# Kernel optimization log

Hardware: AMD Instinct MI355X
Metric: run time of the kernel (lower is better)

## Reference

```python
import jax, jax.numpy as jnp
import numpy as np

HID = 2048      # hidden_size
H = 16          # num query heads
KV = 4          # num kv heads
HD = HID // H   # head_dim = 128
THETA = 1000000.0
T = 2048        # tokens (single causal sequence)


def _rope(x, positions):
    # neox-style rotate-half RoPE over full head_dim. x: [T, h, HD]
    half = HD // 2
    inv_freq = THETA ** (-jnp.arange(half, dtype=jnp.float32) * 2.0 / HD)  # [half]
    freqs = positions.astype(jnp.float32)[:, None] * inv_freq              # [T, half]
    cos = jnp.cos(freqs)[:, None, :]
    sin = jnp.sin(freqs)[:, None, :]
    x1, x2 = x[..., :half], x[..., half:]
    return jnp.concatenate([x1 * cos - x2 * sin, x2 * cos + x1 * sin], axis=-1)


def setup_inputs() -> dict:
    key = jax.random.key(0)
    k1, k2, k3 = jax.random.split(key, 3)
    hidden_states = jax.random.normal(k1, (T, HID), jnp.float32) * 0.02
    w_qkv = jax.random.normal(k2, (HID, (H + 2 * KV) * HD), jnp.float32) * 0.02
    w_o = jax.random.normal(k3, (H * HD, HID), jnp.float32) * 0.02
    positions = jnp.arange(T, dtype=jnp.int32)
    return {"hidden_states": hidden_states, "w_qkv": w_qkv, "w_o": w_o,
            "positions": positions}


def reference(hidden_states, w_qkv, w_o, positions):
    q_size, kv_size = H * HD, KV * HD
    qkv = hidden_states @ w_qkv                                  # [T, q+2kv]
    q = qkv[:, :q_size].reshape(T, H, HD)
    k = qkv[:, q_size:q_size + kv_size].reshape(T, KV, HD)
    v = qkv[:, q_size + kv_size:].reshape(T, KV, HD)
    q = _rope(q, positions)
    k = _rope(k, positions)
    # GQA: expand kv heads to query heads
    group = H // KV
    k_e = jnp.repeat(k, group, axis=1)                           # [T, H, HD]
    v_e = jnp.repeat(v, group, axis=1)
    scale = HD ** -0.5
    scores = jnp.einsum('thd,shd->hts', q, k_e) * scale          # [H, T, T]
    causal = positions[:, None] >= positions[None, :]            # [T, T]
    scores = jnp.where(causal[None, :, :], scores, -1e30)
    attn = jax.nn.softmax(scores, axis=-1)
    o = jnp.einsum('hts,shd->thd', attn, v_e).reshape(T, H * HD)
    return o @ w_o
```

## Files before the change

kernel.cpp:

```cpp
#include <hip/hip_runtime.h>
#include <hip/hip_bf16.h>

#define T_LEN 2048
#define HID 2048
#define NH 16
#define NKV 4
#define HD 128
#define QKV_COLS 3072

typedef __attribute__((ext_vector_type(8))) short bf16x8;
typedef __attribute__((ext_vector_type(4))) float f32x4;

static __device__ __forceinline__ ushort f2bf(float f) {
  __hip_bfloat16 h = __float2bfloat16(f);
  return *reinterpret_cast<ushort*>(&h);
}
static __device__ __forceinline__ float bf2f(ushort u) {
  union { unsigned int i; float f; } v;
  v.i = ((unsigned int)u) << 16;
  return v.f;
}

static __device__ __forceinline__ void async_copy16(const ushort* g, ushort* l) {
  __builtin_amdgcn_global_load_lds(
      (const __attribute__((address_space(1))) unsigned int*)g,
      (__attribute__((address_space(3))) unsigned int*)l, 16, 0, 0);
}

__global__ __launch_bounds__(256) void prep(
    const float* __restrict__ hidden, ushort* __restrict__ hb,
    const float* __restrict__ w_qkv, ushort* __restrict__ wqkvT,
    const int* __restrict__ positions, float2* __restrict__ tbl) {
  __shared__ float t[64][65];
  const int b = blockIdx.x;
  const int tid = threadIdx.x;
  if (b < 4096) {
    int idx = (b * 256 + tid) * 4;
    float4 v = *(const float4*)(hidden + idx);
    ushort4 o;
    o.x = f2bf(v.x); o.y = f2bf(v.y); o.z = f2bf(v.z); o.w = f2bf(v.w);
    *(ushort4*)(hb + idx) = o;
  } else if (b < 5632) {
    const int tb = b - 4096;
    const int bk = (tb & 31) * 64, bn = (tb >> 5) * 64;
    const int c = tid & 63;
#pragma unroll
    for (int i = 0; i < 16; ++i) {
      int r = (tid >> 6) + i * 4;
      t[r][c] = w_qkv[(size_t)(bk + r) * QKV_COLS + bn + c];
    }
    __syncthreads();
#pragma unroll
    for (int i = 0; i < 16; ++i) {
      int r = (tid >> 6) + i * 4;
      wqkvT[(size_t)(bn + r) * HID + bk + c] = f2bf(t[c][r]);
    }
  } else {
    const int rb = b - 5632;
    const int tt = rb * 4 + (tid >> 6), j = tid & 63;
    double inv_freq = pow(1000000.0, -(double)(2 * j) / 128.0);
    double ang = (double)positions[tt] * inv_freq;
    double s, c2;
    sincos(ang, &s, &c2);
    tbl[(size_t)tt * 64 + j] = make_float2((float)c2, (float)s);
  }
}

__global__ __launch_bounds__(256) void transpose_cast(
    const float* __restrict__ W, ushort* __restrict__ WT, int K, int N) {
  __shared__ float t[64][65];
  const int bk = blockIdx.x * 64, bn = blockIdx.y * 64;
  const int tid = threadIdx.x;
  const int c = tid & 63;
#pragma unroll
  for (int i = 0; i < 16; ++i) {
    int r = (tid >> 6) + i * 4;
    t[r][c] = W[(size_t)(bk + r) * N + bn + c];
  }
  __syncthreads();
#pragma unroll
  for (int i = 0; i < 16; ++i) {
    int r = (tid >> 6) + i * 4;
    WT[(size_t)(bn + r) * K + bk + c] = f2bf(t[c][r]);
  }
}

template <bool OUT_BF16>
__global__ __launch_bounds__(256, 3) void gemm_bt(
    const ushort* __restrict__ A, const ushort* __restrict__ BT,
    void* __restrict__ C, int M, int N, int K) {
  __shared__ __align__(16) ushort lds[2][1536 * 8];
  const int tid = threadIdx.x;
  const int bm = blockIdx.y * 64, bn = blockIdx.x * 128;
  const int wave = tid >> 6, lane = tid & 63;
  const int lr = lane & 15, lq = lane >> 4;
  const int wm = (wave & 1) * 32, wn = (wave >> 1) * 64;

  f32x4 acc[2][4];
#pragma unroll
  for (int i = 0; i < 2; ++i)
#pragma unroll
    for (int j = 0; j < 4; ++j) {
      acc[i][j][0] = 0.f; acc[i][j][1] = 0.f;
      acc[i][j][2] = 0.f; acc[i][j][3] = 0.f;
    }

  auto stage = [&](int k0, int buf) {
#pragma unroll
    for (int it = 0; it < 2; ++it) {
      int c = it * 256 + tid;
      int row = c >> 3, sl = c & 7, kc = sl ^ (row & 7);
      async_copy16(A + (size_t)(bm + row) * K + k0 + kc * 8, &lds[buf][c * 8]);
    }
#pragma unroll
    for (int it = 0; it < 4; ++it) {
      int c = it * 256 + tid;
      int row = c >> 3, sl = c & 7, kc = sl ^ (row & 7);
      async_copy16(BT + (size_t)(bn + row) * K + k0 + kc * 8,
                   &lds[buf][(512 + c) * 8]);
    }
  };

  stage(0, 0);
  __syncthreads();
  int cur = 0;
  for (int k0 = 0; k0 < K; k0 += 64) {
    if (k0 + 64 < K) stage(k0 + 64, cur ^ 1);
#pragma unroll
    for (int ks = 0; ks < 2; ++ks) {
      bf16x8 af[2], bfr[4];
#pragma unroll
      for (int mi = 0; mi < 2; ++mi) {
        int row = wm + mi * 16 + lr, kc = ks * 4 + lq;
        af[mi] = *(const bf16x8*)&lds[cur][(row * 8 + (kc ^ (row & 7))) * 8];
      }
#pragma unroll
      for (int ni = 0; ni < 4; ++ni) {
        int row = wn + ni * 16 + lr, kc = ks * 4 + lq;
        bfr[ni] =
            *(const bf16x8*)&lds[cur][(512 + row * 8 + (kc ^ (row & 7))) * 8];
      }
#pragma unroll
      for (int mi = 0; mi < 2; ++mi)
#pragma unroll
        for (int ni = 0; ni < 4; ++ni)
          acc[mi][ni] = __builtin_amdgcn_mfma_f32_16x16x32_bf16(
              af[mi], bfr[ni], acc[mi][ni], 0, 0, 0);
    }
    __syncthreads();
    cur ^= 1;
  }

#pragma unroll
  for (int mi = 0; mi < 2; ++mi)
#pragma unroll
    for (int ni = 0; ni < 4; ++ni)
#pragma unroll
      for (int r = 0; r < 4; ++r) {
        size_t row = bm + wm + mi * 16 + lq * 4 + r;
        size_t col = bn + wn + ni * 16 + lr;
        if (OUT_BF16)
          ((ushort*)C)[row * N + col] = f2bf(acc[mi][ni][r]);
        else
          ((float*)C)[row * N + col] = acc[mi][ni][r];
      }
}

__global__ __launch_bounds__(256, 3) void gemm_qkv(
    const ushort* __restrict__ A, const ushort* __restrict__ BT,
    ushort* __restrict__ qkvb, ushort* __restrict__ vt,
    const float2* __restrict__ tbl, int M, int N, int K) {
  __shared__ __align__(16) ushort lds[2][1536 * 8];
  const int tid = threadIdx.x;
  const int bm = blockIdx.y * 64, bn = blockIdx.x * 128;
  const int wave = tid >> 6, lane = tid & 63;
  const int lr = lane & 15, lq = lane >> 4;
  const int wm = (wave & 1) * 32, wn = (wave >> 1) * 64;

  f32x4 acc[2][4];
#pragma unroll
  for (int i = 0; i < 2; ++i)
#pragma unroll
    for (int j = 0; j < 4; ++j) {
      acc[i][j][0] = 0.f; acc[i][j][1] = 0.f;
      acc[i][j][2] = 0.f; acc[i][j][3] = 0.f;
    }

  auto stage = [&](int k0, int buf) {
#pragma unroll
    for (int it = 0; it < 2; ++it) {
      int c = it * 256 + tid;
      int row = c >> 3, sl = c & 7, kc = sl ^ (row & 7);
      async_copy16(A + (size_t)(bm + row) * K + k0 + kc * 8, &lds[buf][c * 8]);
    }
#pragma unroll
    for (int it = 0; it < 4; ++it) {
      int c = it * 256 + tid;
      int row = c >> 3, sl = c & 7, kc = sl ^ (row & 7);
      async_copy16(BT + (size_t)(bn + row) * K + k0 + kc * 8,
                   &lds[buf][(512 + c) * 8]);
    }
  };

  stage(0, 0);
  __syncthreads();
  int cur = 0;
  for (int k0 = 0; k0 < K; k0 += 64) {
    if (k0 + 64 < K) stage(k0 + 64, cur ^ 1);
#pragma unroll
    for (int ks = 0; ks < 2; ++ks) {
      bf16x8 af[2], bfr[4];
#pragma unroll
      for (int mi = 0; mi < 2; ++mi) {
        int row = wm + mi * 16 + lr, kc = ks * 4 + lq;
        af[mi] = *(const bf16x8*)&lds[cur][(row * 8 + (kc ^ (row & 7))) * 8];
      }
#pragma unroll
      for (int ni = 0; ni < 4; ++ni) {
        int row = wn + ni * 16 + lr, kc = ks * 4 + lq;
        bfr[ni] =
            *(const bf16x8*)&lds[cur][(512 + row * 8 + (kc ^ (row & 7))) * 8];
      }
#pragma unroll
      for (int mi = 0; mi < 2; ++mi)
#pragma unroll
        for (int ni = 0; ni < 4; ++ni)
          acc[mi][ni] = __builtin_amdgcn_mfma_f32_16x16x32_bf16(
              af[mi], bfr[ni], acc[mi][ni], 0, 0, 0);
    }
    __syncthreads();
    cur ^= 1;
  }

  const int head = bn >> 7;
  ushort* ep = &lds[0][0];
  if (head < 20) {
#pragma unroll
    for (int mi = 0; mi < 2; ++mi)
#pragma unroll
      for (int ni = 0; ni < 4; ++ni)
#pragma unroll
        for (int r = 0; r < 4; ++r)
          ep[(wm + mi * 16 + lq * 4 + r) * 130 + wn + ni * 16 + lr] =
              f2bf(acc[mi][ni][r]);
    __syncthreads();

    const float qs = (head < NH) ? 0.08838834764831845f : 1.0f;
#pragma unroll
    for (int it = 0; it < 16; ++it) {
      int idx = it * 256 + tid;
      int row = idx >> 6, j = idx & 63;
      float x1 = bf2f(ep[row * 130 + j]);
      float x2 = bf2f(ep[row * 130 + 64 + j]);
      float2 cs = tbl[(size_t)(bm + row) * 64 + j];
      qkvb[(size_t)(bm + row) * QKV_COLS + bn + j] =
          f2bf((x1 * cs.x - x2 * cs.y) * qs);
      qkvb[(size_t)(bm + row) * QKV_COLS + bn + 64 + j] =
          f2bf((x2 * cs.x + x1 * cs.y) * qs);
    }
  } else {
#pragma unroll
    for (int mi = 0; mi < 2; ++mi)
#pragma unroll
      for (int ni = 0; ni < 4; ++ni)
#pragma unroll
        for (int r = 0; r < 4; ++r)
          ep[(wm + mi * 16 + lq * 4 + r) * 130 + wn + ni * 16 + lr] =
              f2bf(acc[mi][ni][r]);
    __syncthreads();

    const int vd0 = bn - 2560;
#pragma unroll
    for (int it = 0; it < 8; ++it) {
      int idx = it * 256 + tid;
      int vd = idx >> 4, tg = (idx & 15) * 4;
      ushort4 w;
      w.x = ep[(tg + 0) * 130 + vd];
      w.y = ep[(tg + 1) * 130 + vd];
      w.z = ep[(tg + 2) * 130 + vd];
      w.w = ep[(tg + 3) * 130 + vd];
      *(ushort4*)&vt[(size_t)(vd0 + vd) * T_LEN + bm + tg] = w;
    }
  }
}

__global__ __launch_bounds__(256, 3) void attn_mfma(
    const ushort* __restrict__ qkv, const ushort* __restrict__ vt,
    ushort* __restrict__ o, ushort* __restrict__ partials,
    float* __restrict__ ml) {
  int qt, h, k_begin, k_end, slot = -1;
  {
    const int i = blockIdx.x;
    if (i < 512) {
      qt = 31 - (i >> 5);
      const int rem = i & 31;
      h = rem >> 1;
      const int chunk = rem & 1;
      const int n = qt + 1, half = n >> 1;
      k_begin = chunk ? half : 0;
      k_end = chunk ? n : half;
      slot = ((qt - 16) * 16 + h) * 2 + chunk;
    } else {
      const int j = i - 512;
      qt = 15 - (j >> 4);
      h = j & 15;
      k_begin = 0;
      k_end = qt + 1;
    }
  }
  const int kh = h >> 2;
  const int tid = threadIdx.x;
  const int wave = tid >> 6, lane = tid & 63;
  const int lr = lane & 15, lq = lane >> 4;
  const int wq = wave >> 1, ws = wave & 1;

  __shared__ __align__(16) ushort KsL[1024 * 8];
  __shared__ __align__(16) ushort VtsL[1024 * 8];
  __shared__ __align__(16) ushort Ps[8 * 67 * 8];
  __shared__ float l_sh[64][2];

  bf16x8 qf[2][4];
  {
    const ushort* qbase =
        qkv + (size_t)(qt * 64 + wq * 32 + lr) * QKV_COLS + h * HD + lq * 8;
#pragma unroll
    for (int mi = 0; mi < 2; ++mi)
#pragma unroll
      for (int kk = 0; kk < 4; ++kk)
        qf[mi][kk] = *(const bf16x8*)(qbase + (size_t)mi * 16 * QKV_COLS + kk * 32);
  }

  float l_part[2][4];
#pragma unroll
  for (int mi = 0; mi < 2; ++mi)
#pragma unroll
    for (int r = 0; r < 4; ++r) l_part[mi][r] = 0.f;
  f32x4 o_acc[4][2];
#pragma unroll
  for (int qi = 0; qi < 4; ++qi)
#pragma unroll
    for (int di = 0; di < 2; ++di) {
      o_acc[qi][di][0] = 0.f; o_acc[qi][di][1] = 0.f;
      o_acc[qi][di][2] = 0.f; o_acc[qi][di][3] = 0.f;
    }

  for (int kt = k_begin; kt < k_end; ++kt) {
    __syncthreads();

    {
      const ushort* kbase = qkv + 2048 + kh * HD;
#pragma unroll
      for (int it = 0; it < 4; ++it) {
        int c = it * 256 + tid;
        int s = c >> 4, sl = c & 15, dg = sl ^ (s & 15);
        async_copy16(kbase + (size_t)(kt * 64 + s) * QKV_COLS + dg * 8,
                     &KsL[c * 8]);
      }
    }
    {
      const ushort* vbase = vt + (size_t)(kh * HD) * T_LEN + kt * 64;
#pragma unroll
      for (int it = 0; it < 4; ++it) {
        int c = it * 256 + tid;
        int d = c >> 3, sl = c & 7, sc = sl ^ (d & 7);
        async_copy16(vbase + (size_t)d * T_LEN + sc * 8, &VtsL[c * 8]);
      }
    }
    __syncthreads();

    f32x4 s_acc[2][2];
#pragma unroll
    for (int mi = 0; mi < 2; ++mi)
#pragma unroll
      for (int ni = 0; ni < 2; ++ni) {
        s_acc[mi][ni][0] = 0.f; s_acc[mi][ni][1] = 0.f;
        s_acc[mi][ni][2] = 0.f; s_acc[mi][ni][3] = 0.f;
      }
    __builtin_amdgcn_s_setprio(1);
#pragma unroll
    for (int kk = 0; kk < 4; ++kk) {
      bf16x8 kf[2];
#pragma unroll
      for (int ni = 0; ni < 2; ++ni) {
        int s = ws * 32 + ni * 16 + lr;
        kf[ni] = *(const bf16x8*)&KsL[(s * 16 + ((kk * 4 + lq) ^ (s & 15))) * 8];
      }
#pragma unroll
      for (int mi = 0; mi < 2; ++mi)
#pragma unroll
        for (int ni = 0; ni < 2; ++ni)
          s_acc[mi][ni] = __builtin_amdgcn_mfma_f32_16x16x32_bf16(
              qf[mi][kk], kf[ni], s_acc[mi][ni], 0, 0, 0);
    }
    __builtin_amdgcn_s_setprio(0);

    if (kt == qt) {
#pragma unroll
      for (int mi = 0; mi < 2; ++mi)
#pragma unroll
        for (int ni = 0; ni < 2; ++ni)
#pragma unroll
          for (int r = 0; r < 4; ++r)
            if (ws * 32 + ni * 16 + lr > wq * 32 + mi * 16 + lq * 4 + r)
              s_acc[mi][ni][r] = -1e30f;
    }

#pragma unroll
    for (int mi = 0; mi < 2; ++mi)
#pragma unroll
      for (int ni = 0; ni < 2; ++ni)
#pragma unroll
        for (int r = 0; r < 4; ++r) {
          float p = __expf(s_acc[mi][ni][r]);
          l_part[mi][r] += p;
          int s = ws * 32 + ni * 16 + lr;
          int q = wq * 32 + mi * 16 + lq * 4 + r;
          Ps[((s >> 3) * 67 + q) * 8 + (s & 7)] = f2bf(p);
        }
    __syncthreads();

    __builtin_amdgcn_s_setprio(1);
#pragma unroll
    for (int ss = 0; ss < 2; ++ss) {
      bf16x8 vf[2];
#pragma unroll
      for (int di = 0; di < 2; ++di) {
        int d = wave * 32 + di * 16 + lr, sc = ss * 4 + lq;
        vf[di] = *(const bf16x8*)&VtsL[(d * 8 + (sc ^ (d & 7))) * 8];
      }
#pragma unroll
      for (int qi = 0; qi < 4; ++qi) {
        bf16x8 pf = *(const bf16x8*)&Ps[((ss * 4 + lq) * 67 + qi * 16 + lr) * 8];
#pragma unroll
        for (int di = 0; di < 2; ++di)
          o_acc[qi][di] = __builtin_amdgcn_mfma_f32_16x16x32_bf16(
              pf, vf[di], o_acc[qi][di], 0, 0, 0);
      }
    }
    __builtin_amdgcn_s_setprio(0);
  }

#pragma unroll
  for (int mi = 0; mi < 2; ++mi)
#pragma unroll
    for (int r = 0; r < 4; ++r) {
      float v = l_part[mi][r];
#pragma unroll
      for (int off = 1; off < 16; off <<= 1) v += __shfl_xor(v, off, 16);
      l_part[mi][r] = v;
    }
  if (lr == 0) {
#pragma unroll
    for (int mi = 0; mi < 2; ++mi)
#pragma unroll
      for (int r = 0; r < 4; ++r)
        l_sh[wq * 32 + mi * 16 + lq * 4 + r][ws] = l_part[mi][r];
  }
  __syncthreads();

  if (slot < 0) {
    ushort* ob = o + (size_t)(qt * 64) * (NH * HD) + h * HD + wave * 32;
#pragma unroll
    for (int qi = 0; qi < 4; ++qi)
#pragma unroll
      for (int r = 0; r < 4; ++r) {
        int q = qi * 16 + lq * 4 + r;
        float inv = 1.f / (l_sh[q][0] + l_sh[q][1]);
#pragma unroll
        for (int di = 0; di < 2; ++di)
          ob[(size_t)q * (NH * HD) + di * 16 + lr] =
              f2bf(o_acc[qi][di][r] * inv);
      }
  } else {
    ushort* pb = partials + (size_t)slot * 64 * HD + wave * 32;
#pragma unroll
    for (int qi = 0; qi < 4; ++qi)
#pragma unroll
      for (int r = 0; r < 4; ++r) {
        int q = qi * 16 + lq * 4 + r;
#pragma unroll
        for (int di = 0; di < 2; ++di)
          pb[(size_t)q * HD + di * 16 + lr] = f2bf(o_acc[qi][di][r]);
      }
    if (tid < 64) ml[(size_t)slot * 64 + tid] = l_sh[tid][0] + l_sh[tid][1];
  }
}

__global__ __launch_bounds__(256) void attn_reduce(
    const ushort* __restrict__ partials, const float* __restrict__ ml,
    ushort* __restrict__ o) {
  const int bi = blockIdx.x;
  const int qt = 16 + (bi >> 4), h = bi & 15;
  const int s0 = ((qt - 16) * 16 + h) * 2;
  const int tid = threadIdx.x;
  const int row = tid >> 2;
  const int dq = (tid & 3) * 32;

  float l0 = ml[(size_t)s0 * 64 + row];
  float l1 = ml[(size_t)(s0 + 1) * 64 + row];
  float inv = 1.f / (l0 + l1);

  const ushort* p0 = partials + ((size_t)s0 * 64 + row) * HD + dq;
  const ushort* p1 = partials + ((size_t)(s0 + 1) * 64 + row) * HD + dq;
  ushort* ob = o + (size_t)(qt * 64 + row) * (NH * HD) + h * HD + dq;
#pragma unroll
  for (int v = 0; v < 4; ++v) {
    bf16x8 a = *(const bf16x8*)(p0 + v * 8);
    bf16x8 b = *(const bf16x8*)(p1 + v * 8);
    bf16x8 w;
#pragma unroll
    for (int k = 0; k < 8; ++k)
      w[k] = (short)f2bf((bf2f((ushort)a[k]) + bf2f((ushort)b[k])) * inv);
    *(bf16x8*)(ob + v * 8) = w;
  }
}

extern "C" void kernel_launch(void* const* d_in, const int* in_sizes, int n_in,
                              void* d_out, int out_size, void* d_ws,
                              size_t ws_size, hipStream_t stream) {
  const float* hidden = (const float*)d_in[0];
  const float* w_qkv  = (const float*)d_in[1];
  const float* w_o    = (const float*)d_in[2];
  const int* positions = (const int*)d_in[3];
  float* out = (float*)d_out;

  ushort* ws = (ushort*)d_ws;
  ushort* hb    = ws;
  ushort* wqkvT = ws + 4194304;
  ushort* qkvb  = wqkvT + 6291456;
  ushort* vtb   = qkvb + 6291456;
  float*  mlb   = (float*)(vtb + 1048576);
  float2* tbl   = (float2*)(mlb + 32768);
  ushort* ob       = hb;
  ushort* partials = wqkvT;
  ushort* woT      = wqkvT;

  prep<<<6144, 256, 0, stream>>>(hidden, hb, w_qkv, wqkvT, positions, tbl);

  gemm_qkv<<<dim3(QKV_COLS / 128, T_LEN / 64), 256, 0, stream>>>(
      hb, wqkvT, qkvb, vtb, tbl, T_LEN, QKV_COLS, HID);

  attn_mfma<<<768, 256, 0, stream>>>(qkvb, vtb, ob, partials, mlb);
  attn_reduce<<<256, 256, 0, stream>>>(partials, mlb, ob);

  transpose_cast<<<dim3(HID / 64, HID / 64), 256, 0, stream>>>(
      w_o, woT, HID, HID);

  gemm_bt<false><<<dim3(HID / 128, T_LEN / 64), 256, 0, stream>>>(
      ob, woT, out, T_LEN, HID, NH * HD);
}
```

Baseline: 203.4 us.

## Rebalance causal attention split-K into 1/2/3 chunks and fold w_o transpose into prep

Attention work is redistributed so short query tiles run unsplit, middle tiles split the key range in two, and the longest tiles split it in three. The reduce kernel is generalised to sum a variable number of partials. The aim is to even out per-block work across the causal triangle and cut the tail. Separately, when the workspace is large enough, the w_o transpose-cast is folded into the prep kernel as extra blocks, which removes one launch at the cost of more workspace and some extra partial traffic.

After: 197.9 us (median of 2 runs). 2.7% less time.

```diff
diff --git a/kernel.cpp b/kernel.cpp
--- a/kernel.cpp
+++ b/kernel.cpp
@@ -30,7 +30,8 @@
 __global__ __launch_bounds__(256) void prep(
     const float* __restrict__ hidden, ushort* __restrict__ hb,
     const float* __restrict__ w_qkv, ushort* __restrict__ wqkvT,
-    const int* __restrict__ positions, float2* __restrict__ tbl) {
+    const int* __restrict__ positions, float2* __restrict__ tbl,
+    const float* __restrict__ w_o, ushort* __restrict__ woT) {
   __shared__ float t[64][65];
   const int b = blockIdx.x;
   const int tid = threadIdx.x;
@@ -55,7 +56,7 @@
       int r = (tid >> 6) + i * 4;
       wqkvT[(size_t)(bn + r) * HID + bk + c] = f2bf(t[c][r]);
     }
-  } else {
+  } else if (b < 6144) {
     const int rb = b - 5632;
     const int tt = rb * 4 + (tid >> 6), j = tid & 63;
     double inv_freq = pow(1000000.0, -(double)(2 * j) / 128.0);
@@ -63,6 +64,21 @@
     double s, c2;
     sincos(ang, &s, &c2);
     tbl[(size_t)tt * 64 + j] = make_float2((float)c2, (float)s);
+  } else {
+    const int tb = b - 6144;
+    const int bk = (tb & 31) * 64, bn = (tb >> 5) * 64;
+    const int c = tid & 63;
+#pragma unroll
+    for (int i = 0; i < 16; ++i) {
+      int r = (tid >> 6) + i * 4;
+      t[r][c] = w_o[(size_t)(bk + r) * HID + bn + c];
+    }
+    __syncthreads();
+#pragma unroll
+    for (int i = 0; i < 16; ++i) {
+      int r = (tid >> 6) + i * 4;
+      woT[(size_t)(bn + r) * HID + bk + c] = f2bf(t[c][r]);
+    }
   }
 }
 
@@ -291,22 +307,28 @@
   int qt, h, k_begin, k_end, slot = -1;
   {
     const int i = blockIdx.x;
-    if (i < 512) {
-      qt = 31 - (i >> 5);
-      const int rem = i & 31;
-      h = rem >> 1;
-      const int chunk = rem & 1;
-      const int n = qt + 1, half = n >> 1;
-      k_begin = chunk ? half : 0;
-      k_end = chunk ? n : half;
-      slot = ((qt - 16) * 16 + h) * 2 + chunk;
+    int c = 0, nc = 1;
+    if (i < 64) {
+      qt = 11 - (i >> 4); h = i & 15;
+    } else if (i < 448) {
+      int j = i - 64;
+      qt = 23 - (j >> 5);
+      int rem = j & 31;
+      h = rem >> 1; c = rem & 1; nc = 2;
+      slot = ((qt - 12) * 16 + h) * 2 + c;
+    } else if (i < 832) {
+      int j = i - 448;
+      qt = 31 - (j / 48);
+      int rem = j % 48;
+      h = rem / 3; c = rem % 3; nc = 3;
+      slot = 384 + ((qt - 24) * 16 + h) * 3 + c;
     } else {
-      const int j = i - 512;
-      qt = 15 - (j >> 4);
-      h = j & 15;
-      k_begin = 0;
-      k_end = qt + 1;
-    }
+      int j = i - 832;
+      qt = 7 - (j >> 4); h = j & 15;
+    }
+    const int n = qt + 1;
+    k_begin = (n * c) / nc;
+    k_end = (n * (c + 1)) / nc;
   }
   const int kh = h >> 2;
   const int tid = threadIdx.x;
@@ -490,27 +512,42 @@
     const ushort* __restrict__ partials, const float* __restrict__ ml,
     ushort* __restrict__ o) {
   const int bi = blockIdx.x;
-  const int qt = 16 + (bi >> 4), h = bi & 15;
-  const int s0 = ((qt - 16) * 16 + h) * 2;
+  int qt, h, base, cnt;
+  if (bi < 192) {
+    qt = 12 + (bi >> 4); h = bi & 15;
+    base = ((qt - 12) * 16 + h) * 2; cnt = 2;
+  } else {
+    int k = bi - 192;
+    qt = 24 + (k >> 4); h = k & 15;
+    base = 384 + ((qt - 24) * 16 + h) * 3; cnt = 3;
+  }
   const int tid = threadIdx.x;
   const int row = tid >> 2;
   const int dq = (tid & 3) * 32;
 
-  float l0 = ml[(size_t)s0 * 64 + row];
-  float l1 = ml[(size_t)(s0 + 1) * 64 + row];
-  float inv = 1.f / (l0 + l1);
-
-  const ushort* p0 = partials + ((size_t)s0 * 64 + row) * HD + dq;
-  const ushort* p1 = partials + ((size_t)(s0 + 1) * 64 + row) * HD + dq;
+  float lsum = 0.f;
+  for (int c = 0; c < cnt; ++c) lsum += ml[(size_t)(base + c) * 64 + row];
+  const float inv = 1.f / lsum;
+
+  float accf[32];
+#pragma unroll
+  for (int k = 0; k < 32; ++k) accf[k] = 0.f;
+  for (int c = 0; c < cnt; ++c) {
+    const ushort* p = partials + ((size_t)(base + c) * 64 + row) * HD + dq;
+#pragma unroll
+    for (int v = 0; v < 4; ++v) {
+      bf16x8 a = *(const bf16x8*)(p + v * 8);
+#pragma unroll
+      for (int k = 0; k < 8; ++k) accf[v * 8 + k] += bf2f((ushort)a[k]);
+    }
+  }
   ushort* ob = o + (size_t)(qt * 64 + row) * (NH * HD) + h * HD + dq;
 #pragma unroll
   for (int v = 0; v < 4; ++v) {
-    bf16x8 a = *(const bf16x8*)(p0 + v * 8);
-    bf16x8 b = *(const bf16x8*)(p1 + v * 8);
     bf16x8 w;
 #pragma unroll
     for (int k = 0; k < 8; ++k)
-      w[k] = (short)f2bf((bf2f((ushort)a[k]) + bf2f((ushort)b[k])) * inv);
+      w[k] = (short)f2bf(accf[v * 8 + k] * inv);
     *(bf16x8*)(ob + v * 8) = w;
   }
 }
@@ -530,21 +567,27 @@
   ushort* qkvb  = wqkvT + 6291456;
   ushort* vtb   = qkvb + 6291456;
   float*  mlb   = (float*)(vtb + 1048576);
-  float2* tbl   = (float2*)(mlb + 32768);
+  float2* tbl   = (float2*)(mlb + 49152);
+  ushort* wsend = (ushort*)(tbl + 131072);
   ushort* ob       = hb;
   ushort* partials = wqkvT;
-  ushort* woT      = wqkvT;
-
-  prep<<<6144, 256, 0, stream>>>(hidden, hb, w_qkv, wqkvT, positions, tbl);
+
+  const size_t need_bytes = (18448384ull + 4194304ull) * 2;
+  const bool fast = ws_size >= need_bytes;
+  ushort* woT = fast ? wsend : wqkvT;
+
+  prep<<<fast ? 7168 : 6144, 256, 0, stream>>>(
+      hidden, hb, w_qkv, wqkvT, positions, tbl, w_o, woT);
 
   gemm_qkv<<<dim3(QKV_COLS / 128, T_LEN / 64), 256, 0, stream>>>(
       hb, wqkvT, qkvb, vtb, tbl, T_LEN, QKV_COLS, HID);
 
-  attn_mfma<<<768, 256, 0, stream>>>(qkvb, vtb, ob, partials, mlb);
-  attn_reduce<<<256, 256, 0, stream>>>(partials, mlb, ob);
-
-  transpose_cast<<<dim3(HID / 64, HID / 64), 256, 0, stream>>>(
-      w_o, woT, HID, HID);
+  attn_mfma<<<960, 256, 0, stream>>>(qkvb, vtb, ob, partials, mlb);
+  attn_reduce<<<320, 256, 0, stream>>>(partials, mlb, ob);
+
+  if (!fast)
+    transpose_cast<<<dim3(HID / 64, HID / 64), 256, 0, stream>>>(
+        w_o, woT, HID, HID);
 
   gemm_bt<false><<<dim3(HID / 128, T_LEN / 64), 256, 0, stream>>>(
       ob, woT, out, T_LEN, HID, NH * HD);
```
